# Optimization experiments

Measured on AMD Instinct MI355X. Metric: run time of the kernel, lower is better.

Reference implementation:

```python
import jax, jax.numpy as jnp
import numpy as np

F8_MAX = 448.0  # max representable value of float8_e4m3fn


def setup_inputs() -> dict:
    key = jax.random.key(0)
    k1, k2, k3 = jax.random.split(key, 3)
    inp = jax.random.normal(k1, (4, 2048, 4096), dtype=jnp.float32)
    weight = jax.random.normal(k2, (4096, 16384), dtype=jnp.float32) * 0.02  # [in, out] (stored transposed)
    bias = jax.random.normal(k3, (16384,), dtype=jnp.float32)
    return {"inp": inp, "weight": weight, "bias": bias}


def reference(inp, weight, bias):
    # --- weight quantization (from_float with abs-max observer) ---
    w_scale = jnp.max(jnp.abs(weight)) / F8_MAX                      # scalar fp32
    w_q = (weight * (1.0 / w_scale)).astype(jnp.float8_e4m3fn)       # [in, out] fp8

    # --- dynamic input quantization: amax = max(|min|, |max|) ---
    x = inp.reshape(-1, inp.shape[-1])                               # [N, in]
    amax = jnp.maximum(jnp.abs(jnp.min(x)), jnp.abs(jnp.max(x)))
    x_scale = amax / F8_MAX
    x_q = (x * (1.0 / x_scale)).astype(jnp.float8_e4m3fn)            # [N, in] fp8

    # --- fp8_gemm_v2: dequant-matmul with fused scales + bias ---
    out = jnp.matmul(x_q.astype(jnp.float32), w_q.astype(jnp.float32))
    out = out * (x_scale * w_scale) + bias                           # [N, out]
    return out.reshape(inp.shape[:-1] + (weight.shape[1],))
```

## Files before the change

### kernel.cpp

```cpp
#include <hip/hip_runtime.h>
#include <stdint.h>
#include <stddef.h>

typedef float f32x16 __attribute__((ext_vector_type(16)));
typedef int i32x8 __attribute__((ext_vector_type(8)));

union Frag32 { long l[4]; i32x8 v; };


__global__ void absmax_kernel(const float4* __restrict__ x, size_t n4,
                              unsigned int* __restrict__ out) {
  size_t idx = ((size_t)blockIdx.x * blockDim.x + threadIdx.x) * 2;
  size_t stride = (size_t)gridDim.x * blockDim.x * 2;
  float m0 = 0.f, m1 = 0.f;
  for (size_t i = idx; i < n4; i += stride) {
    float4 v = x[i];
    float4 u = x[i + 1];
    m0 = fmaxf(m0, fmaxf(fmaxf(fabsf(v.x), fabsf(v.y)),
                         fmaxf(fabsf(v.z), fabsf(v.w))));
    m1 = fmaxf(m1, fmaxf(fmaxf(fabsf(u.x), fabsf(u.y)),
                         fmaxf(fabsf(u.z), fabsf(u.w))));
  }
  float m = fmaxf(m0, m1);
#pragma unroll
  for (int off = 32; off > 0; off >>= 1)
    m = fmaxf(m, __shfl_xor(m, off));
  if ((threadIdx.x & 63) == 0)
    atomicMax(out, __float_as_uint(m));
}

__global__ void quantize_x_kernel(const float4* __restrict__ x,
                                  uint8_t* __restrict__ xq,
                                  const unsigned int* __restrict__ amax,
                                  int K, int n_chunks) {
  const float x_scale = __uint_as_float(amax[1]) / 448.0f;
  const float inv = 1.0f / x_scale;
  const int kslots = K >> 5;
  int idx = blockIdx.x * blockDim.x + threadIdx.x;
  const int stride = gridDim.x * blockDim.x;
  for (; idx < n_chunks; idx += stride) {
    const int slot = idx >> 9;
    const int p16 = idx & 511;
    const int row = p16 >> 1;
    const int kkb0 = (p16 & 1) << 4;
    const int mblk = slot / kslots;
    const int ksl = slot - mblk * kslots;
    const size_t f4 = ((size_t)(mblk * 256 + row) * K + ksl * 32 + kkb0) >> 2;
    const float4 v0 = x[f4 + 0], v1 = x[f4 + 1], v2 = x[f4 + 2], v3 = x[f4 + 3];
    uint32_t c0 = __builtin_amdgcn_cvt_pk_fp8_f32(v0.x * inv, v0.y * inv, 0, false);
    c0 = __builtin_amdgcn_cvt_pk_fp8_f32(v0.z * inv, v0.w * inv, c0, true);
    uint32_t c1 = __builtin_amdgcn_cvt_pk_fp8_f32(v1.x * inv, v1.y * inv, 0, false);
    c1 = __builtin_amdgcn_cvt_pk_fp8_f32(v1.z * inv, v1.w * inv, c1, true);
    uint32_t c2 = __builtin_amdgcn_cvt_pk_fp8_f32(v2.x * inv, v2.y * inv, 0, false);
    c2 = __builtin_amdgcn_cvt_pk_fp8_f32(v2.z * inv, v2.w * inv, c2, true);
    uint32_t c3 = __builtin_amdgcn_cvt_pk_fp8_f32(v3.x * inv, v3.y * inv, 0, false);
    c3 = __builtin_amdgcn_cvt_pk_fp8_f32(v3.z * inv, v3.w * inv, c3, true);
    const unsigned long long L0 = (unsigned long long)c0 | ((unsigned long long)c1 << 32);
    const unsigned long long L1 = (unsigned long long)c2 | ((unsigned long long)c3 << 32);
    const int Lc = row * 32 + kkb0;
    const int mask = ((row >> 2) & 3) << 3;
    const int addr0 = Lc ^ (mask & 16);
    uint8_t* p = xq + (size_t)slot * 8192;
    *(unsigned long long*)(p + addr0 + (mask & 8)) = L0;
    *(unsigned long long*)(p + addr0 + (8 ^ (mask & 8))) = L1;
  }
}

__global__ void quantize_wT_kernel(const float* __restrict__ w,
                                   uint8_t* __restrict__ wqt,
                                   const unsigned int* __restrict__ amax,
                                   int N, int K) {
  __shared__ float tileF[64][129];
  const float w_scale = __uint_as_float(amax[0]) / 448.0f;
  const float inv = 1.0f / w_scale;
  const int tn = blockIdx.x;
  const int tk = blockIdx.y;
  const int t = threadIdx.x;
  {
    const int nn4 = t & 15;
    const int kk0 = t >> 4;
#pragma unroll
    for (int i = 0; i < 8; ++i) {
      const int kk = kk0 + i * 16;
      const float4 v =
          *(const float4*)&w[(size_t)(tk * 128 + kk) * N + tn * 64 + nn4 * 4];
      tileF[nn4 * 4 + 0][kk] = v.x;
      tileF[nn4 * 4 + 1][kk] = v.y;
      tileF[nn4 * 4 + 2][kk] = v.z;
      tileF[nn4 * 4 + 3][kk] = v.w;
    }
  }
  __syncthreads();
  {
    const int n = t & 63;
    const int c = t >> 6;
    unsigned long long q[4];
#pragma unroll
    for (int cc = 0; cc < 4; ++cc) {
      const float4 u0 = *(const float4*)&tileF[n][c * 32 + cc * 8];
      const float4 u1 = *(const float4*)&tileF[n][c * 32 + cc * 8 + 4];
      uint32_t lo = __builtin_amdgcn_cvt_pk_fp8_f32(u0.x * inv, u0.y * inv, 0, false);
      lo = __builtin_amdgcn_cvt_pk_fp8_f32(u0.z * inv, u0.w * inv, lo, true);
      uint32_t hi = __builtin_amdgcn_cvt_pk_fp8_f32(u1.x * inv, u1.y * inv, 0, false);
      hi = __builtin_amdgcn_cvt_pk_fp8_f32(u1.z * inv, u1.w * inv, hi, true);
      q[cc] = (unsigned long long)lo | ((unsigned long long)hi << 32);
    }
    const int n_g = tn * 64 + n;
    const int k0g = tk * 128 + c * 32;
    const size_t slot = (size_t)(n_g >> 8) * (K >> 5) + (k0g >> 5);
    const int row = n_g & 255;
    const int mask = (row >> 2) & 3;
    ulonglong2 s0, s1;
    s0.x = q[0 ^ mask]; s0.y = q[1 ^ mask];
    s1.x = q[2 ^ mask]; s1.y = q[3 ^ mask];
    uint8_t* pbase = wqt + slot * 8192 + row * 32;
    *(ulonglong2*)(pbase) = s0;
    *(ulonglong2*)(pbase + 16) = s1;
  }
}

#define T_BM 256
#define T_BN 256
#define UNIT_SCALE 0x7F7F7F7F

__device__ __forceinline__ void gl_lds16(const uint8_t* g, uint8_t* lds) {
  __builtin_amdgcn_global_load_lds(
      (const __attribute__((address_space(1))) void*)g,
      (__attribute__((address_space(3))) void*)lds, 16, 0, 0);
}

__global__ __launch_bounds__(512, 2) void gemm_fp8_mx(
    const uint8_t* __restrict__ Aq, const uint8_t* __restrict__ BqT,
    const float* __restrict__ bias, const unsigned int* __restrict__ amax,
    float* __restrict__ C, int M, int N, int K) {
  extern __shared__ uint8_t smem[];
  uint8_t* const Ar = smem;
  uint8_t* const Br = smem + 65536;

  const int ntn = N / T_BN;
  const int bid = blockIdx.x;
  const int m0 = (bid / ntn) * T_BM;
  const int n0 = (bid % ntn) * T_BN;

  const int tid = threadIdx.x;
  const int w = tid >> 6;
  const int l = tid & 63;
  const int wr = w >> 1;
  const int wc = w & 1;

  const int kslots = K >> 5;

  const int soff = w * 2048 + l * 16;
  const uint8_t* a_src = Aq + (size_t)(m0 >> 8) * kslots * 8192 + soff;
  const uint8_t* b_src = BqT + (size_t)(n0 >> 8) * kslots * 8192 + soff;

  const int h = l >> 5;
  const int rl = l & 31;
  int aoff[2][4], boff[4][4];
#pragma unroll
  for (int mt = 0; mt < 2; ++mt) {
    const int ra = wr * 64 + mt * 32 + rl;
#pragma unroll
    for (int j = 0; j < 4; ++j)
      aoff[mt][j] = h * 8192 + ra * 32 + ((j ^ ((ra >> 2) & 3)) * 8);
  }
#pragma unroll
  for (int nt = 0; nt < 4; ++nt) {
    const int rb = wc * 128 + nt * 32 + rl;
#pragma unroll
    for (int j = 0; j < 4; ++j)
      boff[nt][j] = h * 8192 + rb * 32 + ((j ^ ((rb >> 2) & 3)) * 8);
  }

  f32x16 acc[2][4];
#pragma unroll
  for (int i = 0; i < 2; ++i)
#pragma unroll
    for (int j = 0; j < 4; ++j) acc[i][j] = 0.f;

  const int NP = K >> 6;

#pragma unroll
  for (int sidx = 0; sidx < 2; ++sidx) {
    gl_lds16(a_src + sidx * 16384, Ar + sidx * 16384 + soff);
    gl_lds16(a_src + sidx * 16384 + 1024, Ar + sidx * 16384 + soff + 1024);
    gl_lds16(b_src + sidx * 16384, Br + sidx * 16384 + soff);
    gl_lds16(b_src + sidx * 16384 + 1024, Br + sidx * 16384 + soff + 1024);
  }
  asm volatile("s_waitcnt vmcnt(4)" ::: "memory");
  __builtin_amdgcn_s_barrier();

  for (int p = 0; p < NP; ++p) {
    const int ss = (p + 2 < NP) ? (p + 2) : (p - 2);
    const int rslot = ((p + 2) & 3) * 16384;
    gl_lds16(a_src + (size_t)ss * 16384, Ar + rslot + soff);
    gl_lds16(a_src + (size_t)ss * 16384 + 1024, Ar + rslot + soff + 1024);
    gl_lds16(b_src + (size_t)ss * 16384, Br + rslot + soff);
    gl_lds16(b_src + (size_t)ss * 16384 + 1024, Br + rslot + soff + 1024);

    const uint8_t* Asl = Ar + (p & 3) * 16384;
    const uint8_t* Bsl = Br + (p & 3) * 16384;
    Frag32 af[2], bf[4];
#pragma unroll
    for (int mt = 0; mt < 2; ++mt)
#pragma unroll
      for (int j = 0; j < 4; ++j)
        af[mt].l[j] = *(const long*)(Asl + aoff[mt][j]);
#pragma unroll
    for (int nt = 0; nt < 4; ++nt)
#pragma unroll
      for (int j = 0; j < 4; ++j)
        bf[nt].l[j] = *(const long*)(Bsl + boff[nt][j]);

    __builtin_amdgcn_s_setprio(1);
#pragma unroll
    for (int nt = 0; nt < 4; ++nt) {
      acc[0][nt] = __builtin_amdgcn_mfma_scale_f32_32x32x64_f8f6f4(
          af[0].v, bf[nt].v, acc[0][nt], 0, 0, 0, UNIT_SCALE, 0, UNIT_SCALE);
      acc[1][nt] = __builtin_amdgcn_mfma_scale_f32_32x32x64_f8f6f4(
          af[1].v, bf[nt].v, acc[1][nt], 0, 0, 0, UNIT_SCALE, 0, UNIT_SCALE);
    }
    __builtin_amdgcn_s_setprio(0);

    asm volatile("s_waitcnt vmcnt(4)" ::: "memory");
    __builtin_amdgcn_s_barrier();
  }
  asm volatile("s_waitcnt vmcnt(0)" ::: "memory");

  const float x_scale = __uint_as_float(amax[1]) / 448.0f;
  const float w_scale = __uint_as_float(amax[0]) / 448.0f;
  const float s = x_scale * w_scale;
  const int colb = n0 + wc * 128 + rl;
  const int rowb = m0 + wr * 64 + 4 * h;
#pragma unroll
  for (int nt = 0; nt < 4; ++nt) {
    const int col = colb + nt * 32;
    const float bv = bias[col];
#pragma unroll
    for (int mt = 0; mt < 2; ++mt) {
#pragma unroll
      for (int r = 0; r < 16; ++r) {
        const int row = rowb + mt * 32 + (r & 3) + 8 * (r >> 2);
        C[(size_t)row * N + col] = acc[mt][nt][r] * s + bv;
      }
    }
  }
}

extern "C" void kernel_launch(void* const* d_in, const int* in_sizes, int n_in,
                              void* d_out, int out_size, void* d_ws, size_t ws_size,
                              hipStream_t stream) {
  const float* inp = (const float*)d_in[0];
  const float* weight = (const float*)d_in[1];
  const float* bias = (const float*)d_in[2];
  float* out = (float*)d_out;

  const int N = in_sizes[2];
  const int K = in_sizes[1] / N;
  const int M = in_sizes[0] / K;

  uint8_t* ws = (uint8_t*)d_ws;
  unsigned int* amax = (unsigned int*)ws;
  uint8_t* xq = ws + 256;
  uint8_t* wqt = ws + 256 + (size_t)M * K;

  hipMemsetAsync(d_ws, 0, 8, stream);

  absmax_kernel<<<2048, 256, 0, stream>>>((const float4*)weight,
                                          (size_t)K * N / 4, amax + 0);
  absmax_kernel<<<2048, 256, 0, stream>>>((const float4*)inp,
                                          (size_t)M * K / 4, amax + 1);

  quantize_x_kernel<<<4096, 256, 0, stream>>>((const float4*)inp, xq, amax,
                                              K, M * K / 16);
  quantize_wT_kernel<<<dim3(N / 64, K / 128), 256, 0, stream>>>(weight, wqt,
                                                                amax, N, K);

  gemm_fp8_mx<<<(M / T_BM) * (N / T_BN), 512, 131072, stream>>>(
      xq, wqt, bias, amax, out, M, N, K);
}
```

Measured before the change: 900.3 us.

## Split GEMM tile across sixteen waves with 16-byte LDS swizzle and paired-phase barriers

The fp8 GEMM block grows from 512 to 1024 threads. Each of the 16 waves now computes a 64x64 sub-tile instead of 64x128, and each wave issues one global-to-LDS load per operand per phase. The quantize kernels change the row swizzle to 16-byte granularity so fragments can be read from LDS with 128-bit loads instead of 64-bit ones. The main loop runs two K-phases per barrier to halve barrier count. The aim is more waves to hide latency and fewer LDS instructions, at the cost of less register-level reuse per wave and a tighter register budget. Phase p+1 reads data other waves loaded without an intervening barrier, which could be a synchronisation hazard.

```diff
diff --git a/kernel.cpp b/kernel.cpp
--- a/kernel.cpp
+++ b/kernel.cpp
@@ -55,14 +55,10 @@
     c2 = __builtin_amdgcn_cvt_pk_fp8_f32(v2.z * inv, v2.w * inv, c2, true);
     uint32_t c3 = __builtin_amdgcn_cvt_pk_fp8_f32(v3.x * inv, v3.y * inv, 0, false);
     c3 = __builtin_amdgcn_cvt_pk_fp8_f32(v3.z * inv, v3.w * inv, c3, true);
-    const unsigned long long L0 = (unsigned long long)c0 | ((unsigned long long)c1 << 32);
-    const unsigned long long L1 = (unsigned long long)c2 | ((unsigned long long)c3 << 32);
-    const int Lc = row * 32 + kkb0;
-    const int mask = ((row >> 2) & 3) << 3;
-    const int addr0 = Lc ^ (mask & 16);
-    uint8_t* p = xq + (size_t)slot * 8192;
-    *(unsigned long long*)(p + addr0 + (mask & 8)) = L0;
-    *(unsigned long long*)(p + addr0 + (8 ^ (mask & 8))) = L1;
+    const int paddr = (row * 32 + kkb0) ^ (((row >> 2) & 1) << 4);
+    uint4 o;
+    o.x = c0; o.y = c1; o.z = c2; o.w = c3;
+    *(uint4*)(xq + (size_t)slot * 8192 + paddr) = o;
   }
 }
 
@@ -109,13 +105,13 @@
     const int k0g = tk * 128 + c * 32;
     const size_t slot = (size_t)(n_g >> 8) * (K >> 5) + (k0g >> 5);
     const int row = n_g & 255;
-    const int mask = (row >> 2) & 3;
+    const int bit = (row >> 2) & 1;
+    uint8_t* pbase = wqt + slot * 8192 + row * 32;
     ulonglong2 s0, s1;
-    s0.x = q[0 ^ mask]; s0.y = q[1 ^ mask];
-    s1.x = q[2 ^ mask]; s1.y = q[3 ^ mask];
-    uint8_t* pbase = wqt + slot * 8192 + row * 32;
-    *(ulonglong2*)(pbase) = s0;
-    *(ulonglong2*)(pbase + 16) = s1;
+    s0.x = q[0]; s0.y = q[1];
+    s1.x = q[2]; s1.y = q[3];
+    *(ulonglong2*)(pbase + (bit << 4)) = s0;
+    *(ulonglong2*)(pbase + ((bit ^ 1) << 4)) = s1;
   }
 }
 
@@ -129,7 +125,7 @@
       (__attribute__((address_space(3))) void*)lds, 16, 0, 0);
 }
 
-__global__ __launch_bounds__(512, 2) void gemm_fp8_mx(
+__global__ __launch_bounds__(1024, 4) void gemm_fp8_mx(
     const uint8_t* __restrict__ Aq, const uint8_t* __restrict__ BqT,
     const float* __restrict__ bias, const unsigned int* __restrict__ amax,
     float* __restrict__ C, int M, int N, int K) {
@@ -145,84 +141,79 @@
   const int tid = threadIdx.x;
   const int w = tid >> 6;
   const int l = tid & 63;
-  const int wr = w >> 1;
-  const int wc = w & 1;
+  const int wr = w >> 2;
+  const int wc = w & 3;
 
   const int kslots = K >> 5;
 
-  const int soff = w * 2048 + l * 16;
+  const int soff = w * 1024 + l * 16;
   const uint8_t* a_src = Aq + (size_t)(m0 >> 8) * kslots * 8192 + soff;
   const uint8_t* b_src = BqT + (size_t)(n0 >> 8) * kslots * 8192 + soff;
 
   const int h = l >> 5;
   const int rl = l & 31;
-  int aoff[2][4], boff[4][4];
+  int aoff[2][2], boff[2][2];
 #pragma unroll
   for (int mt = 0; mt < 2; ++mt) {
     const int ra = wr * 64 + mt * 32 + rl;
-#pragma unroll
-    for (int j = 0; j < 4; ++j)
-      aoff[mt][j] = h * 8192 + ra * 32 + ((j ^ ((ra >> 2) & 3)) * 8);
-  }
-#pragma unroll
-  for (int nt = 0; nt < 4; ++nt) {
-    const int rb = wc * 128 + nt * 32 + rl;
-#pragma unroll
-    for (int j = 0; j < 4; ++j)
-      boff[nt][j] = h * 8192 + rb * 32 + ((j ^ ((rb >> 2) & 3)) * 8);
-  }
-
-  f32x16 acc[2][4];
+    const int rb = wc * 64 + mt * 32 + rl;
+#pragma unroll
+    for (int c = 0; c < 2; ++c) {
+      aoff[mt][c] = h * 8192 + ra * 32 + ((c ^ ((ra >> 2) & 1)) << 4);
+      boff[mt][c] = h * 8192 + rb * 32 + ((c ^ ((rb >> 2) & 1)) << 4);
+    }
+  }
+
+  f32x16 acc[2][2];
 #pragma unroll
   for (int i = 0; i < 2; ++i)
 #pragma unroll
-    for (int j = 0; j < 4; ++j) acc[i][j] = 0.f;
+    for (int j = 0; j < 2; ++j) acc[i][j] = 0.f;
 
   const int NP = K >> 6;
 
-#pragma unroll
-  for (int sidx = 0; sidx < 2; ++sidx) {
-    gl_lds16(a_src + sidx * 16384, Ar + sidx * 16384 + soff);
-    gl_lds16(a_src + sidx * 16384 + 1024, Ar + sidx * 16384 + soff + 1024);
-    gl_lds16(b_src + sidx * 16384, Br + sidx * 16384 + soff);
-    gl_lds16(b_src + sidx * 16384 + 1024, Br + sidx * 16384 + soff + 1024);
-  }
-  asm volatile("s_waitcnt vmcnt(4)" ::: "memory");
+  gl_lds16(a_src, Ar + soff);
+  gl_lds16(b_src, Br + soff);
+  gl_lds16(a_src + 16384, Ar + 16384 + soff);
+  gl_lds16(b_src + 16384, Br + 16384 + soff);
+  asm volatile("s_waitcnt vmcnt(2)" ::: "memory");
   __builtin_amdgcn_s_barrier();
 
-  for (int p = 0; p < NP; ++p) {
-    const int ss = (p + 2 < NP) ? (p + 2) : (p - 2);
-    const int rslot = ((p + 2) & 3) * 16384;
-    gl_lds16(a_src + (size_t)ss * 16384, Ar + rslot + soff);
-    gl_lds16(a_src + (size_t)ss * 16384 + 1024, Ar + rslot + soff + 1024);
-    gl_lds16(b_src + (size_t)ss * 16384, Br + rslot + soff);
-    gl_lds16(b_src + (size_t)ss * 16384 + 1024, Br + rslot + soff + 1024);
-
-    const uint8_t* Asl = Ar + (p & 3) * 16384;
-    const uint8_t* Bsl = Br + (p & 3) * 16384;
-    Frag32 af[2], bf[4];
-#pragma unroll
-    for (int mt = 0; mt < 2; ++mt)
-#pragma unroll
-      for (int j = 0; j < 4; ++j)
-        af[mt].l[j] = *(const long*)(Asl + aoff[mt][j]);
-#pragma unroll
-    for (int nt = 0; nt < 4; ++nt)
-#pragma unroll
-      for (int j = 0; j < 4; ++j)
-        bf[nt].l[j] = *(const long*)(Bsl + boff[nt][j]);
-
-    __builtin_amdgcn_s_setprio(1);
-#pragma unroll
-    for (int nt = 0; nt < 4; ++nt) {
-      acc[0][nt] = __builtin_amdgcn_mfma_scale_f32_32x32x64_f8f6f4(
-          af[0].v, bf[nt].v, acc[0][nt], 0, 0, 0, UNIT_SCALE, 0, UNIT_SCALE);
-      acc[1][nt] = __builtin_amdgcn_mfma_scale_f32_32x32x64_f8f6f4(
-          af[1].v, bf[nt].v, acc[1][nt], 0, 0, 0, UNIT_SCALE, 0, UNIT_SCALE);
-    }
-    __builtin_amdgcn_s_setprio(0);
-
-    asm volatile("s_waitcnt vmcnt(4)" ::: "memory");
+#define PHASE_(pp)                                                          \
+  do {                                                                      \
+    const int ss = ((pp) + 2 < NP) ? ((pp) + 2) : ((pp)-2);                 \
+    const int rslot = (((pp) + 2) & 3) * 16384;                             \
+    gl_lds16(a_src + (size_t)ss * 16384, Ar + rslot + soff);                \
+    gl_lds16(b_src + (size_t)ss * 16384, Br + rslot + soff);                \
+    const uint8_t* Asl = Ar + ((pp)&3) * 16384;                             \
+    const uint8_t* Bsl = Br + ((pp)&3) * 16384;                             \
+    Frag32 af[2], bf[2];                                                    \
+    _Pragma("unroll") for (int mt = 0; mt < 2; ++mt) {                      \
+      ulonglong2 ta0 = *(const ulonglong2*)(Asl + aoff[mt][0]);             \
+      ulonglong2 ta1 = *(const ulonglong2*)(Asl + aoff[mt][1]);             \
+      af[mt].l[0] = (long)ta0.x; af[mt].l[1] = (long)ta0.y;                 \
+      af[mt].l[2] = (long)ta1.x; af[mt].l[3] = (long)ta1.y;                 \
+      ulonglong2 tb0 = *(const ulonglong2*)(Bsl + boff[mt][0]);             \
+      ulonglong2 tb1 = *(const ulonglong2*)(Bsl + boff[mt][1]);             \
+      bf[mt].l[0] = (long)tb0.x; bf[mt].l[1] = (long)tb0.y;                 \
+      bf[mt].l[2] = (long)tb1.x; bf[mt].l[3] = (long)tb1.y;                 \
+    }                                                                       \
+    __builtin_amdgcn_s_setprio(1);                                          \
+    acc[0][0] = __builtin_amdgcn_mfma_scale_f32_32x32x64_f8f6f4(            \
+        af[0].v, bf[0].v, acc[0][0], 0, 0, 0, UNIT_SCALE, 0, UNIT_SCALE);   \
+    acc[1][0] = __builtin_amdgcn_mfma_scale_f32_32x32x64_f8f6f4(            \
+        af[1].v, bf[0].v, acc[1][0], 0, 0, 0, UNIT_SCALE, 0, UNIT_SCALE);   \
+    acc[0][1] = __builtin_amdgcn_mfma_scale_f32_32x32x64_f8f6f4(            \
+        af[0].v, bf[1].v, acc[0][1], 0, 0, 0, UNIT_SCALE, 0, UNIT_SCALE);   \
+    acc[1][1] = __builtin_amdgcn_mfma_scale_f32_32x32x64_f8f6f4(            \
+        af[1].v, bf[1].v, acc[1][1], 0, 0, 0, UNIT_SCALE, 0, UNIT_SCALE);   \
+    __builtin_amdgcn_s_setprio(0);                                          \
+    asm volatile("s_waitcnt vmcnt(2)" ::: "memory");                        \
+  } while (0)
+
+  for (int p = 0; p < NP; p += 2) {
+    PHASE_(p);
+    PHASE_(p + 1);
     __builtin_amdgcn_s_barrier();
   }
   asm volatile("s_waitcnt vmcnt(0)" ::: "memory");
@@ -230,10 +221,10 @@
   const float x_scale = __uint_as_float(amax[1]) / 448.0f;
   const float w_scale = __uint_as_float(amax[0]) / 448.0f;
   const float s = x_scale * w_scale;
-  const int colb = n0 + wc * 128 + rl;
+  const int colb = n0 + wc * 64 + rl;
   const int rowb = m0 + wr * 64 + 4 * h;
 #pragma unroll
-  for (int nt = 0; nt < 4; ++nt) {
+  for (int nt = 0; nt < 2; ++nt) {
     const int col = colb + nt * 32;
     const float bv = bias[col];
 #pragma unroll
@@ -276,6 +267,6 @@
   quantize_wT_kernel<<<dim3(N / 64, K / 128), 256, 0, stream>>>(weight, wqt,
                                                                 amax, N, K);
 
-  gemm_fp8_mx<<<(M / T_BM) * (N / T_BN), 512, 131072, stream>>>(
+  gemm_fp8_mx<<<(M / T_BM) * (N / T_BN), 1024, 131072, stream>>>(
       xq, wqt, bias, amax, out, M, N, K);
 }
```

Result: no change. 904.9 us (+0.5%).
